# Performance work log

Hardware: AMD Instinct MI355X
Metric: run time of the kernel (lower is better)

## Reference

```python
import jax, jax.numpy as jnp
import numpy as np

D = 2048  # input_size
H = 2048  # hidden_size
K = 4096  # number of children


def setup_inputs() -> dict:
    key = jax.random.key(0)
    ks = jax.random.split(key, 12)
    sD = 1.0 / np.sqrt(D)
    sH = 1.0 / np.sqrt(H)
    return {
        "input": jax.random.normal(ks[0], (D,), dtype=jnp.float32),
        "children_c": jax.random.normal(ks[1], (K, H), dtype=jnp.float32),
        "children_h": jax.random.normal(ks[2], (K, H), dtype=jnp.float32),
        "W_iou_x": jax.random.uniform(ks[3], (3 * H, D), jnp.float32, -sD, sD),
        "b_iou_x": jax.random.uniform(ks[4], (3 * H,), jnp.float32, -sD, sD),
        "W_iou_h": jax.random.uniform(ks[5], (3 * H, H), jnp.float32, -sH, sH),
        "b_iou_h": jax.random.uniform(ks[6], (3 * H,), jnp.float32, -sH, sH),
        "W_fx": jax.random.uniform(ks[7], (H, D), jnp.float32, -sD, sD),
        "b_fx": jax.random.uniform(ks[8], (H,), jnp.float32, -sD, sD),
        "W_fh": jax.random.uniform(ks[9], (H, H), jnp.float32, -sH, sH),
        "b_fh": jax.random.uniform(ks[10], (H,), jnp.float32, -sH, sH),
    }


def reference(input, children_c, children_h,
              W_iou_x, b_iou_x, W_iou_h, b_iou_h,
              W_fx, b_fx, W_fh, b_fh):
    # iou = iou_x(input) + iou_h(sum_k h_k)  -> [3H]
    h_sum = jnp.sum(children_h, axis=0)
    iou = (W_iou_x @ input + b_iou_x) + (W_iou_h @ h_sum + b_iou_h)
    i, o, u = jnp.split(iou, 3)
    i = jax.nn.sigmoid(i)
    o = jax.nn.sigmoid(o)
    u = jnp.tanh(u)
    # per-child forget gates, batched over K (original loops in Python):
    # f_k = sigmoid(f_x(input) + f_h(h_k))  -> [K, H]
    fx = W_fx @ input + b_fx                       # [H], computed once
    fh = children_h @ W_fh.T + b_fh                # [K, H] GEMM
    f = jax.nn.sigmoid(fx[None, :] + fh)           # [K, H]
    c = i * u + jnp.sum(f * children_c, axis=0)    # [H]
    h = o * jnp.tanh(c)                            # [H]
    return (o, c, h)
```

## Files before the change

### kernel.cpp

```cpp
#include <hip/hip_runtime.h>

typedef unsigned short u16;
typedef short bf16x8 __attribute__((ext_vector_type(8)));
typedef float f32x4 __attribute__((ext_vector_type(4)));

#define D_IN 2048
#define H_DIM 2048
#define K_CH 4096

__device__ __forceinline__ u16 f2bf(float f) {
  unsigned int u = __float_as_uint(f);
  u += 0x7fffu + ((u >> 16) & 1u);
  return (u16)(u >> 16);
}
__device__ __forceinline__ float sigmoidf(float x) {
  return 1.0f / (1.0f + __expf(-x));
}
__device__ __forceinline__ uint4 packrow(float4 a, float4 b) {
  uint4 w;
  w.x = (unsigned)f2bf(a.x) | ((unsigned)f2bf(a.y) << 16);
  w.y = (unsigned)f2bf(a.z) | ((unsigned)f2bf(a.w) << 16);
  w.z = (unsigned)f2bf(b.x) | ((unsigned)f2bf(b.y) << 16);
  w.w = (unsigned)f2bf(b.z) | ((unsigned)f2bf(b.w) << 16);
  return w;
}

__global__ __launch_bounds__(256) void k1(
    const float* __restrict__ ch, const float* __restrict__ wfh,
    const float* __restrict__ Wfx, const float* __restrict__ bfx,
    const float* __restrict__ bfh, const float* __restrict__ x,
    const float* __restrict__ Wix, const float* __restrict__ bix,
    const float* __restrict__ bih, float* __restrict__ partials,
    u16* __restrict__ chb, u16* __restrict__ wfhb, float* __restrict__ g,
    float* __restrict__ ioux, float* __restrict__ hsum,
    float* __restrict__ accv) {
  const int t = threadIdx.x;
  const int bid = blockIdx.x;
  if (bid < 1024) {
    const int r0 = bid * 4;
    float4 a[4], b[4];
#pragma unroll
    for (int r = 0; r < 4; ++r) {
      const float4* p = (const float4*)(ch + (size_t)(r0 + r) * H_DIM + t * 8);
      a[r] = p[0];
      b[r] = p[1];
    }
    float s0 = 0.f, s1 = 0.f, s2 = 0.f, s3 = 0.f;
    float s4 = 0.f, s5 = 0.f, s6 = 0.f, s7 = 0.f;
#pragma unroll
    for (int r = 0; r < 4; ++r) {
      s0 += a[r].x; s1 += a[r].y; s2 += a[r].z; s3 += a[r].w;
      s4 += b[r].x; s5 += b[r].y; s6 += b[r].z; s7 += b[r].w;
      *(uint4*)(chb + (size_t)(r0 + r) * H_DIM + t * 8) = packrow(a[r], b[r]);
    }
    float4 lo, hi;
    lo.x = s0; lo.y = s1; lo.z = s2; lo.w = s3;
    hi.x = s4; hi.y = s5; hi.z = s6; hi.w = s7;
    float* pp = partials + (size_t)bid * H_DIM + t * 8;
    *(float4*)pp = lo;
    *(float4*)(pp + 4) = hi;
  } else if (bid < 1536) {
    const size_t base = (size_t)(bid - 1024) * 8192 + t * 8;
    float4 a[4], b[4];
#pragma unroll
    for (int j = 0; j < 4; ++j) {
      const float4* p = (const float4*)(wfh + base + j * 2048);
      a[j] = p[0];
      b[j] = p[1];
    }
#pragma unroll
    for (int j = 0; j < 4; ++j)
      *(uint4*)(wfhb + base + j * 2048) = packrow(a[j], b[j]);
  } else if (bid < 2048) {
    const int wave = t >> 6, lane = t & 63;
    const int h = (bid - 1536) * 4 + wave;
    const float4* w = (const float4*)(Wfx + (size_t)h * D_IN);
    const float4* xv = (const float4*)x;
    float s = 0.f;
#pragma unroll
    for (int i = 0; i < 8; ++i) {
      int idx = i * 64 + lane;
      float4 av = w[idx], bv = xv[idx];
      s += av.x * bv.x + av.y * bv.y + av.z * bv.z + av.w * bv.w;
    }
#pragma unroll
    for (int off = 32; off > 0; off >>= 1) s += __shfl_xor(s, off);
    if (lane == 0) g[h] = s + bfx[h] + bfh[h];
  } else if (bid < 3584) {
    const int wave = t >> 6, lane = t & 63;
    const int row = (bid - 2048) * 4 + wave;
    const float4* w = (const float4*)(Wix + (size_t)row * D_IN);
    const float4* xv = (const float4*)x;
    float s = 0.f;
#pragma unroll
    for (int i = 0; i < 8; ++i) {
      int idx = i * 64 + lane;
      float4 av = w[idx], bv = xv[idx];
      s += av.x * bv.x + av.y * bv.y + av.z * bv.z + av.w * bv.w;
    }
#pragma unroll
    for (int off = 32; off > 0; off >>= 1) s += __shfl_xor(s, off);
    if (lane == 0) ioux[row] = s + bix[row] + bih[row];
  } else {
    float4 z = {0.f, 0.f, 0.f, 0.f};
    ((float4*)hsum)[t * 2] = z;
    ((float4*)hsum)[t * 2 + 1] = z;
    ((float4*)accv)[t * 2] = z;
    ((float4*)accv)[t * 2 + 1] = z;
  }
}

#define BM 128
#define BN 128
#define BK 64

__global__ __launch_bounds__(256) void kG(
    const u16* __restrict__ chb, const float* __restrict__ cc,
    const u16* __restrict__ wfhb, const float* __restrict__ g,
    const float* __restrict__ partials, float* __restrict__ hsum,
    float* __restrict__ accv) {
  __shared__ u16 As[2][BM * BK];
  __shared__ u16 Bs[2][BN * BK];

  const int bid = blockIdx.x;
  const int t = threadIdx.x;

  if (bid < 64) {
    const int c = (bid & 7) * 256 + t;
    const int p0 = (bid >> 3) * 128;
    float a0 = 0.f, a1 = 0.f, a2 = 0.f, a3 = 0.f;
    float a4 = 0.f, a5 = 0.f, a6 = 0.f, a7 = 0.f;
    for (int p = p0; p < p0 + 128; p += 8) {
      a0 += partials[(size_t)(p + 0) * H_DIM + c];
      a1 += partials[(size_t)(p + 1) * H_DIM + c];
      a2 += partials[(size_t)(p + 2) * H_DIM + c];
      a3 += partials[(size_t)(p + 3) * H_DIM + c];
      a4 += partials[(size_t)(p + 4) * H_DIM + c];
      a5 += partials[(size_t)(p + 5) * H_DIM + c];
      a6 += partials[(size_t)(p + 6) * H_DIM + c];
      a7 += partials[(size_t)(p + 7) * H_DIM + c];
    }
    float s = ((a0 + a1) + (a2 + a3)) + ((a4 + a5) + (a6 + a7));
    atomicAdd(hsum + c, s);
    return;
  }

  const int gb = bid - 64;
  const int wave = t >> 6, lane = t & 63;
  const int lrow = lane & 15, lquad = lane >> 4;
  const int wm = wave >> 1, wn = wave & 1;
  const int row0 = (gb & 31) * BM;
  const int col0 = (gb >> 5) * BN;

  f32x4 acc[4][4] = {};

  const int srow = lane >> 3;
  const int schunk = (lane & 7) ^ srow;
  const u16* agbase = chb  + (size_t)(row0 + wave * 32 + srow) * H_DIM + schunk * 8;
  const u16* bgbase = wfhb + (size_t)(col0 + wave * 32 + srow) * H_DIM + schunk * 8;

#define STAGE(buf, kb)                                                        \
  do {                                                                        \
    _Pragma("unroll")                                                         \
    for (int i = 0; i < 4; ++i)                                               \
      __builtin_amdgcn_global_load_lds(                                       \
          (const __attribute__((address_space(1))) void*)(agbase + (size_t)i * 8 * H_DIM + (kb) * BK), \
          (__attribute__((address_space(3))) void*)(&As[buf][(wave * 32 + i * 8) * 64]), \
          16, 0, 0);                                                          \
    _Pragma("unroll")                                                         \
    for (int i = 0; i < 4; ++i)                                               \
      __builtin_amdgcn_global_load_lds(                                       \
          (const __attribute__((address_space(1))) void*)(bgbase + (size_t)i * 8 * H_DIM + (kb) * BK), \
          (__attribute__((address_space(3))) void*)(&Bs[buf][(wave * 32 + i * 8) * 64]), \
          16, 0, 0);                                                          \
  } while (0)

#define COMPUTE(buf)                                                          \
  do {                                                                        \
    _Pragma("unroll")                                                         \
    for (int step = 0; step < 2; ++step) {                                    \
      const int slot = ((step * 4 + lquad) ^ (lrow & 7)) * 8;                 \
      bf16x8 fa[4], fb[4];                                                    \
      _Pragma("unroll")                                                       \
      for (int i = 0; i < 4; ++i)                                             \
        fa[i] = *(const bf16x8*)(&As[buf][(wm * 64 + i * 16 + lrow) * 64 + slot]); \
      _Pragma("unroll")                                                       \
      for (int i = 0; i < 4; ++i)                                             \
        fb[i] = *(const bf16x8*)(&Bs[buf][(wn * 64 + i * 16 + lrow) * 64 + slot]); \
      _Pragma("unroll")                                                       \
      for (int mi = 0; mi < 4; ++mi)                                          \
        _Pragma("unroll")                                                     \
        for (int ni = 0; ni < 4; ++ni)                                        \
          acc[mi][ni] = __builtin_amdgcn_mfma_f32_16x16x32_bf16(              \
              fa[mi], fb[ni], acc[mi][ni], 0, 0, 0);                          \
    }                                                                         \
  } while (0)

  STAGE(0, 0);
  __syncthreads();

  for (int kb = 0; kb < D_IN / BK - 1; ++kb) {
    const int cur = kb & 1;
    STAGE(cur ^ 1, kb + 1);
    COMPUTE(cur);
    __syncthreads();
  }
  COMPUTE(1);

#pragma unroll
  for (int ni = 0; ni < 4; ++ni) {
    const int colg = col0 + wn * 64 + ni * 16 + lrow;
    const float gv = g[colg];
    float s = 0.f;
#pragma unroll
    for (int mi = 0; mi < 4; ++mi) {
      const int rowg = row0 + wm * 64 + mi * 16 + lquad * 4;
#pragma unroll
      for (int r = 0; r < 4; ++r) {
        float f = sigmoidf(gv + acc[mi][ni][r]);
        s += f * cc[(size_t)(rowg + r) * H_DIM + colg];
      }
    }
    s += __shfl_xor(s, 16);
    s += __shfl_xor(s, 32);
    if (lquad == 0) atomicAdd(accv + colg, s);
  }
#undef STAGE
#undef COMPUTE
}

__global__ __launch_bounds__(256) void kmv2(const float* __restrict__ Wih,
                                            const float* __restrict__ hsum,
                                            float* __restrict__ iou) {
  const int wave = threadIdx.x >> 6, lane = threadIdx.x & 63;
  const int row = blockIdx.x * 4 + wave;
  const float4* w = (const float4*)(Wih + (size_t)row * H_DIM);
  const float4* hv = (const float4*)hsum;
  float s = 0.f;
#pragma unroll
  for (int i = 0; i < 8; ++i) {
    int idx = i * 64 + lane;
    float4 a = w[idx], b = hv[idx];
    s += a.x * b.x + a.y * b.y + a.z * b.z + a.w * b.w;
  }
#pragma unroll
  for (int off = 32; off > 0; off >>= 1) s += __shfl_xor(s, off);
  if (lane == 0) iou[row] += s;
}

__global__ __launch_bounds__(256) void kfinal(const float* __restrict__ iou,
                                              const float* __restrict__ accv,
                                              float* __restrict__ out) {
  const int h = blockIdx.x * 256 + threadIdx.x;
  float si = sigmoidf(iou[h]);
  float so = sigmoidf(iou[H_DIM + h]);
  float tu = tanhf(iou[2 * H_DIM + h]);
  float c = si * tu + accv[h];
  float hh = so * tanhf(c);
  out[h] = so;
  out[H_DIM + h] = c;
  out[2 * H_DIM + h] = hh;
}

extern "C" void kernel_launch(void* const* d_in, const int* in_sizes, int n_in,
                              void* d_out, int out_size, void* d_ws, size_t ws_size,
                              hipStream_t stream) {
  const float* x   = (const float*)d_in[0];
  const float* cc  = (const float*)d_in[1];
  const float* ch  = (const float*)d_in[2];
  const float* Wix = (const float*)d_in[3];
  const float* bix = (const float*)d_in[4];
  const float* Wih = (const float*)d_in[5];
  const float* bih = (const float*)d_in[6];
  const float* Wfx = (const float*)d_in[7];
  const float* bfx = (const float*)d_in[8];
  const float* Wfh = (const float*)d_in[9];
  const float* bfh = (const float*)d_in[10];

  float* ws   = (float*)d_ws;
  float* hsum = ws;
  float* iou  = ws + 2048;
  float* g    = ws + 8192;
  float* accv = ws + 10240;
  float* partials = ws + 12288;
  u16* chb  = (u16*)(ws + 12288 + 1024 * 2048);
  u16* wfhb = chb + (size_t)K_CH * H_DIM;
  float* out = (float*)d_out;

  k1<<<3585, 256, 0, stream>>>(ch, Wfh, Wfx, bfx, bfh, x, Wix, bix, bih,
                               partials, chb, wfhb, g, iou, hsum, accv);
  kG<<<576, 256, 0, stream>>>(chb, cc, wfhb, g, partials, hsum, accv);
  kmv2<<<1536, 256, 0, stream>>>(Wih, hsum, iou);
  kfinal<<<8, 256, 0, stream>>>(iou, accv, out);
}
```

Before: 264.7 us.

## Enlarge GEMM tiles to 256x128 with 512 threads, XCD-aware mapping, fuse final kernel

```diff
diff --git a/kernel.cpp b/kernel.cpp
--- a/kernel.cpp
+++ b/kernel.cpp
@@ -33,7 +33,7 @@
     const float* __restrict__ bih, float* __restrict__ partials,
     u16* __restrict__ chb, u16* __restrict__ wfhb, float* __restrict__ g,
     float* __restrict__ ioux, float* __restrict__ hsum,
-    float* __restrict__ accv) {
+    float* __restrict__ accv, float* __restrict__ ticket) {
   const int t = threadIdx.x;
   const int bid = blockIdx.x;
   if (bid < 1024) {
@@ -107,14 +107,15 @@
     ((float4*)hsum)[t * 2 + 1] = z;
     ((float4*)accv)[t * 2] = z;
     ((float4*)accv)[t * 2 + 1] = z;
-  }
-}
-
-#define BM 128
+    if (t < 64) ((float4*)ticket)[t] = z;
+  }
+}
+
+#define BM 256
 #define BN 128
 #define BK 64
 
-__global__ __launch_bounds__(256) void kG(
+__global__ __launch_bounds__(512) void kG(
     const u16* __restrict__ chb, const float* __restrict__ cc,
     const u16* __restrict__ wfhb, const float* __restrict__ g,
     const float* __restrict__ partials, float* __restrict__ hsum,
@@ -126,11 +127,11 @@
   const int t = threadIdx.x;
 
   if (bid < 64) {
-    const int c = (bid & 7) * 256 + t;
-    const int p0 = (bid >> 3) * 128;
+    const int c = (bid & 7) * 256 + (t & 255);
+    const int p0 = (bid >> 3) * 128 + (t >> 8) * 64;
     float a0 = 0.f, a1 = 0.f, a2 = 0.f, a3 = 0.f;
     float a4 = 0.f, a5 = 0.f, a6 = 0.f, a7 = 0.f;
-    for (int p = p0; p < p0 + 128; p += 8) {
+    for (int p = p0; p < p0 + 64; p += 8) {
       a0 += partials[(size_t)(p + 0) * H_DIM + c];
       a1 += partials[(size_t)(p + 1) * H_DIM + c];
       a2 += partials[(size_t)(p + 2) * H_DIM + c];
@@ -146,18 +147,23 @@
   }
 
   const int gb = bid - 64;
+  const int xcd = gb & 7;
+  const int u = gb >> 3;
+  const int bm = (xcd << 1) | (u >> 4);
+  const int bn = u & 15;
+  const int row0 = bm * BM;
+  const int col0 = bn * BN;
+
   const int wave = t >> 6, lane = t & 63;
   const int lrow = lane & 15, lquad = lane >> 4;
   const int wm = wave >> 1, wn = wave & 1;
-  const int row0 = (gb & 31) * BM;
-  const int col0 = (gb >> 5) * BN;
 
   f32x4 acc[4][4] = {};
 
   const int srow = lane >> 3;
   const int schunk = (lane & 7) ^ srow;
   const u16* agbase = chb  + (size_t)(row0 + wave * 32 + srow) * H_DIM + schunk * 8;
-  const u16* bgbase = wfhb + (size_t)(col0 + wave * 32 + srow) * H_DIM + schunk * 8;
+  const u16* bgbase = wfhb + (size_t)(col0 + wave * 16 + srow) * H_DIM + schunk * 8;
 
 #define STAGE(buf, kb)                                                        \
   do {                                                                        \
@@ -168,10 +174,10 @@
           (__attribute__((address_space(3))) void*)(&As[buf][(wave * 32 + i * 8) * 64]), \
           16, 0, 0);                                                          \
     _Pragma("unroll")                                                         \
-    for (int i = 0; i < 4; ++i)                                               \
+    for (int i = 0; i < 2; ++i)                                               \
       __builtin_amdgcn_global_load_lds(                                       \
           (const __attribute__((address_space(1))) void*)(bgbase + (size_t)i * 8 * H_DIM + (kb) * BK), \
-          (__attribute__((address_space(3))) void*)(&Bs[buf][(wave * 32 + i * 8) * 64]), \
+          (__attribute__((address_space(3))) void*)(&Bs[buf][(wave * 16 + i * 8) * 64]), \
           16, 0, 0);                                                          \
   } while (0)
 
@@ -229,10 +235,14 @@
 #undef COMPUTE
 }
 
-__global__ __launch_bounds__(256) void kmv2(const float* __restrict__ Wih,
+__global__ __launch_bounds__(256) void kmv3(const float* __restrict__ Wih,
                                             const float* __restrict__ hsum,
-                                            float* __restrict__ iou) {
-  const int wave = threadIdx.x >> 6, lane = threadIdx.x & 63;
+                                            float* __restrict__ iou,
+                                            const float* __restrict__ accv,
+                                            float* __restrict__ ticket,
+                                            float* __restrict__ out) {
+  const int t = threadIdx.x;
+  const int wave = t >> 6, lane = t & 63;
   const int row = blockIdx.x * 4 + wave;
   const float4* w = (const float4*)(Wih + (size_t)row * H_DIM);
   const float4* hv = (const float4*)hsum;
@@ -246,20 +256,28 @@
 #pragma unroll
   for (int off = 32; off > 0; off >>= 1) s += __shfl_xor(s, off);
   if (lane == 0) iou[row] += s;
-}
-
-__global__ __launch_bounds__(256) void kfinal(const float* __restrict__ iou,
-                                              const float* __restrict__ accv,
-                                              float* __restrict__ out) {
-  const int h = blockIdx.x * 256 + threadIdx.x;
-  float si = sigmoidf(iou[h]);
-  float so = sigmoidf(iou[H_DIM + h]);
-  float tu = tanhf(iou[2 * H_DIM + h]);
-  float c = si * tu + accv[h];
-  float hh = so * tanhf(c);
-  out[h] = so;
-  out[H_DIM + h] = c;
-  out[2 * H_DIM + h] = hh;
+
+  __threadfence();
+  __syncthreads();
+  __shared__ int lastflag;
+  if (t == 0) {
+    unsigned int v = atomicAdd((unsigned int*)ticket, 1u);
+    lastflag = (v == (unsigned int)(gridDim.x - 1));
+  }
+  __syncthreads();
+  if (lastflag) {
+    __threadfence();
+    for (int h = t; h < H_DIM; h += 256) {
+      float si = sigmoidf(iou[h]);
+      float so = sigmoidf(iou[H_DIM + h]);
+      float tu = tanhf(iou[2 * H_DIM + h]);
+      float c = si * tu + accv[h];
+      float hh = so * tanhf(c);
+      out[h] = so;
+      out[H_DIM + h] = c;
+      out[2 * H_DIM + h] = hh;
+    }
+  }
 }
 
 extern "C" void kernel_launch(void* const* d_in, const int* in_sizes, int n_in,
@@ -282,14 +300,14 @@
   float* iou  = ws + 2048;
   float* g    = ws + 8192;
   float* accv = ws + 10240;
-  float* partials = ws + 12288;
-  u16* chb  = (u16*)(ws + 12288 + 1024 * 2048);
+  float* ticket = ws + 12288;
+  float* partials = ws + 12544;
+  u16* chb  = (u16*)(ws + 12544 + 1024 * 2048);
   u16* wfhb = chb + (size_t)K_CH * H_DIM;
   float* out = (float*)d_out;
 
   k1<<<3585, 256, 0, stream>>>(ch, Wfh, Wfx, bfx, bfh, x, Wix, bix, bih,
-                               partials, chb, wfhb, g, iou, hsum, accv);
-  kG<<<576, 256, 0, stream>>>(chb, cc, wfhb, g, partials, hsum, accv);
-  kmv2<<<1536, 256, 0, stream>>>(Wih, hsum, iou);
-  kfinal<<<8, 256, 0, stream>>>(iou, accv, out);
-}
+                               partials, chb, wfhb, g, iou, hsum, accv, ticket);
+  kG<<<320, 512, 0, stream>>>(chb, cc, wfhb, g, partials, hsum, accv);
+  kmv3<<<1536, 256, 0, stream>>>(Wih, hsum, iou, accv, ticket, out);
+}
```

After: 454.7 us. 1.72x slower.
